# Performance work log

Hardware: AMD Instinct MI355X
Metric: run time of the kernel (lower is better)

## Reference

```python
import jax, jax.numpy as jnp
import numpy as np
from jax import lax


def setup_inputs() -> dict:
    key = jax.random.key(0)
    k1, k2, k3 = jax.random.split(key, 3)
    B, H, W_, C = 2, 384, 1280, 3
    F = 32
    return {
        "xl": jax.random.normal(k1, (B, H, W_, C), dtype=jnp.float32),
        "xr": jax.random.normal(k2, (B, H, W_, C), dtype=jnp.float32),
        "W": jax.random.normal(k3, (3, 3, C, F), dtype=jnp.float32) * 0.1,
        "b": jnp.zeros((F,), dtype=jnp.float32),
        "num_disparity": 96,
    }


def _features(x, W, b):
    # stand-in for the pretrained backbone: 3x3 stride-2 conv + relu (channels_last)
    f = lax.conv_general_dilated(x, W, window_strides=(2, 2), padding="SAME",
                                 dimension_numbers=("NHWC", "HWIO", "NHWC"))
    return jax.nn.relu(f + b)


def reference(xl, xr, W, b, num_disparity):
    D = num_disparity
    x = jnp.concatenate([xl, xr], axis=0)            # [2B,H,W,3]
    f = _features(x, W, b)                            # [2B,H/2,W/2,F]
    f = jax.image.resize(f, (f.shape[0], f.shape[1] * 2, f.shape[2] * 2, f.shape[3]),
                         method="bilinear")          # [2B,H,W,F]
    fl, fr = jnp.split(f, 2, axis=0)                  # each [B,H,W,F]

    # plane-sweep cost volume: sum over channels of squared diff vs width-rolled right features
    def step(_, d):
        cost_d = jnp.sum((fl - jnp.roll(fr, d, axis=2)) ** 2, axis=-1)  # [B,H,W]
        return None, cost_d

    _, cost = lax.scan(step, None, jnp.arange(D))     # [D,B,H,W]

    s = -177.0 * cost / jnp.max(cost, axis=0, keepdims=True)
    w = jax.nn.softmax(s, axis=0)
    disp_idx = jnp.arange(D, dtype=w.dtype)[:, None, None, None]
    return jnp.sum(disp_idx * w, axis=0)              # [B,H,W]
```

## Files before the change

### kernel.cpp

```cpp
#include <hip/hip_runtime.h>
#include <cstddef>

typedef _Float16 h2    __attribute__((ext_vector_type(2)));
typedef _Float16 half8 __attribute__((ext_vector_type(8)));
typedef float    f32x4 __attribute__((ext_vector_type(4)));

#define CH    192
#define CWID  640
#define IMG_H 384
#define IMG_W 1280
#define TW    128
#define GR    224
#define RAWC  179
#define RAWP  192

__device__ __forceinline__ float fastrcp(float x) {
#if __has_builtin(__builtin_amdgcn_rcpf)
  return __builtin_amdgcn_rcpf(x);
#else
  return 1.0f / x;
#endif
}
__device__ __forceinline__ float fastexp2(float x) {
#if __has_builtin(__builtin_amdgcn_exp2f)
  return __builtin_amdgcn_exp2f(x);
#else
  return exp2f(x);
#endif
}
__device__ __forceinline__ float swz16(float x) {
  return __uint_as_float((unsigned)__builtin_amdgcn_ds_swizzle((int)__float_as_uint(x), 0x401F));
}
__device__ __forceinline__ float bperm(int addr, float x) {
  return __uint_as_float((unsigned)__builtin_amdgcn_ds_bpermute(addr, (int)__float_as_uint(x)));
}

__global__ __launch_bounds__(256)
void conv_relu_kernel(const float* __restrict__ xl, const float* __restrict__ xr,
                      const float* __restrict__ Wt, const float* __restrict__ bias,
                      _Float16* __restrict__ Fc) {
  __shared__ float wl[864];
  __shared__ float bl[32];
  const int tid = threadIdx.x;
  for (int t = tid; t < 864; t += 256) wl[t] = Wt[t];
  if (tid < 32) bl[tid] = bias[tid];
  __syncthreads();

  const int g  = blockIdx.x * 256 + tid;
  const int ow = g % CWID;
  const int t2 = g / CWID;
  const int oh = t2 % CH;
  const int bb = t2 / CH;
  const float* src = (bb < 2) ? (xl + (size_t)bb * IMG_H * IMG_W * 3)
                              : (xr + (size_t)(bb - 2) * IMG_H * IMG_W * 3);
  float acc[32];
  #pragma unroll
  for (int c = 0; c < 32; ++c) acc[c] = bl[c];

  #pragma unroll
  for (int kh = 0; kh < 3; ++kh) {
    const int ir = oh * 2 + kh;
    if (ir >= IMG_H) continue;
    #pragma unroll
    for (int kw = 0; kw < 3; ++kw) {
      const int ic = ow * 2 + kw;
      if (ic >= IMG_W) continue;
      const float* px = src + ((size_t)ir * IMG_W + ic) * 3;
      #pragma unroll
      for (int ci = 0; ci < 3; ++ci) {
        const float v = px[ci];
        const float* wp = &wl[((kh * 3 + kw) * 3 + ci) * 32];
        #pragma unroll
        for (int c8 = 0; c8 < 8; ++c8) {
          const float4 w4 = *(const float4*)(wp + c8 * 4);
          acc[c8 * 4 + 0] = fmaf(v, w4.x, acc[c8 * 4 + 0]);
          acc[c8 * 4 + 1] = fmaf(v, w4.y, acc[c8 * 4 + 1]);
          acc[c8 * 4 + 2] = fmaf(v, w4.z, acc[c8 * 4 + 2]);
          acc[c8 * 4 + 3] = fmaf(v, w4.w, acc[c8 * 4 + 3]);
        }
      }
    }
  }
  _Float16 hv[32];
  #pragma unroll
  for (int c = 0; c < 32; ++c) hv[c] = (_Float16)fmaxf(acc[c], 0.f);
  half8* dst = (half8*)(Fc + (size_t)g * 32);
  #pragma unroll
  for (int q = 0; q < 4; ++q) {
    half8 o;
    #pragma unroll
    for (int e = 0; e < 8; ++e) o[e] = hv[q * 8 + e];
    dst[q] = o;
  }
}

__global__ __launch_bounds__(256, 4)
void disparity_mfma_kernel(const _Float16* __restrict__ Fc, float* __restrict__ out) {
  __shared__ alignas(16) _Float16 raw[RAWP * 32];
  __shared__ alignas(16) _Float16 flH[8 * 512];
  __shared__ alignas(16) _Float16 gH[14 * 512];
  __shared__ alignas(16) float As[TW];
  __shared__ alignas(16) float Bs[GR];

  const int tid = threadIdx.x;
  const int w0  = blockIdx.x * TW;
  const int h   = blockIdx.y;
  const int bz  = blockIdx.z;

  const int hk = h >> 1;
  int r0, r1; float wv0;
  if (h & 1) { r0 = hk; r1 = (hk + 1 > CH - 1) ? CH - 1 : hk + 1; wv0 = 0.75f; }
  else       { r0 = (hk - 1 < 0) ? 0 : hk - 1; r1 = hk;           wv0 = 0.25f; }
  const half8 w0v = (half8)(_Float16)wv0;
  const half8 w1v = (half8)(_Float16)(1.0f - wv0);

  const int vbaseL = (w0 >> 1) + 639;
  const int vbaseR = (w0 >> 1) + 592;

  char* const rawB = (char*)raw;

  const char* const bL0 = (const char*)(Fc + ((size_t)bz * CH + r0) * CWID * 32);
  const char* const bL1 = (const char*)(Fc + ((size_t)bz * CH + r1) * CWID * 32);
  const char* const bR0 = (const char*)(Fc + ((size_t)(bz + 2) * CH + r0) * CWID * 32);
  const char* const bR1 = (const char*)(Fc + ((size_t)(bz + 2) * CH + r1) * CWID * 32);

  #pragma unroll
  for (int it = 0; it < 3; ++it) {
    const int task = tid + it * 256;
    const int t    = task >> 2;
    const int tc   = (t > RAWC - 1) ? RAWC - 1 : t;
    const int c16  = task & 3;
    const bool isfl = tc < 66;
    int v = isfl ? (vbaseL + tc) : (vbaseR + tc - 66);
    v -= (v >= 640) ? 640 : 0;
    v -= (v >= 640) ? 640 : 0;
    const char* p0 = isfl ? bL0 : bR0;
    const char* p1 = isfl ? bL1 : bR1;
    const int off = (v << 6) + (c16 << 4);
    const half8 a0 = *(const half8*)(p0 + off);
    const half8 a1 = *(const half8*)(p1 + off);
    const half8 vv = a0 * w0v + a1 * w1v;
    *(half8*)(rawB + t * 64 + ((c16 ^ (t & 3)) << 4)) = vv;
  }
  __syncthreads();

  const _Float16 h75 = (_Float16)0.75f, h25 = (_Float16)0.25f;
  auto row_body = [&](int row) {
    const bool isfl = row < TW;
    const int r  = isfl ? row : row - TW;
    const int uv = isfl ? (w0 + r) : (w0 - 95 + r);
    const int uact = uv < 0 ? uv + IMG_W : (uv >= IMG_W ? uv - IMG_W : uv);
    const int up = uv + IMG_W;
    const int vm0 = (up - 1) >> 1;
    int t0 = vm0 - (isfl ? vbaseL : (vbaseR - 66));
    int t1 = t0 + 1;
    if (uact == 0)         t0 = t1;
    if (uact == IMG_W - 1) t1 = t0;
    const _Float16 hw0 = (up & 1) ? h75 : h25;
    const _Float16 hw1 = (up & 1) ? h25 : h75;
    const half8 h0v = (half8)hw0;
    const half8 h1v = (half8)hw1;
    const char* r0p = rawB + t0 * 64;
    const char* r1p = rawB + t1 * 64;
    const int k0s = t0 & 3, k1s = t1 & 3;
    const int rr  = r & 15;
    char* dstB = (char*)(isfl ? flH : gH) + (r >> 4) * 1024 + rr * 64;
    float s = 0.f;
    #pragma unroll
    for (int c16 = 0; c16 < 4; ++c16) {
      const half8 a = *(const half8*)(r0p + ((c16 ^ k0s) << 4));
      const half8 b = *(const half8*)(r1p + ((c16 ^ k1s) << 4));
      const half8 v = a * h0v + b * h1v;
      #pragma unroll
      for (int e = 0; e < 4; ++e) {
        h2 pe = {v[2 * e], v[2 * e + 1]};
#if __has_builtin(__builtin_amdgcn_fdot2)
        s = __builtin_amdgcn_fdot2(pe, pe, s, false);
#else
        s += (float)pe[0] * (float)pe[0] + (float)pe[1] * (float)pe[1];
#endif
      }
      *(half8*)(dstB + ((c16 ^ (rr & 3)) << 4)) = v;
    }
    if (isfl) As[r] = s; else Bs[r] = s;
  };
  row_body(tid);
  if (tid < TW + GR - 256) row_body(tid + 256);
  __syncthreads();

  const int lane = tid & 63;
  const int wid  = tid >> 6;
  const int n  = lane & 15;
  const int gq = lane >> 4;
  const int foffB = n * 64 + ((gq ^ (n & 3)) << 4);
  const int bpaddr = (lane ^ 32) << 2;

  #pragma unroll
  for (int pp = 0; pp < 2; ++pp) {
    const int p = wid * 2 + pp;
    const half8 bfrag = *(const half8*)((const char*)flH + p * 1024 + foffB);
    f32x4 acc[7];
    #pragma unroll
    for (int dq = 0; dq < 7; ++dq) {
      const half8 afrag = *(const half8*)((const char*)gH + (p + dq) * 1024 + foffB);
      f32x4 z = {0.f, 0.f, 0.f, 0.f};
      acc[dq] = __builtin_amdgcn_mfma_f32_16x16x32_f16(afrag, bfrag, z, 0, 0, 0);
    }

    const float Ai = As[p * 16 + n];
    float cv[7][4];
    float mn = 3.0e38f, mx = -3.0e38f;
    #pragma unroll
    for (int dq = 0; dq < 7; ++dq) {
      const f32x4 b4 = *(const f32x4*)(&Bs[(p + dq) * 16 + gq * 4]);
      float cm[4], cx[4];
      #pragma unroll
      for (int rg = 0; rg < 4; ++rg) {
        const int m = gq * 4 + rg;
        const float cc = fmaf(-2.f, acc[dq][rg], Ai + b4[rg]);
        const bool valid = (dq != 0 || m >= n) && (dq != 6 || m < n);
        cm[rg] = valid ? cc : 3.0e38f;
        cx[rg] = valid ? cc : -3.0e38f;
        cv[dq][rg] = cm[rg];
      }
      mn = fminf(mn, fminf(fminf(cm[0], cm[1]), fminf(cm[2], cm[3])));
      mx = fmaxf(mx, fmaxf(fmaxf(cx[0], cx[1]), fmaxf(cx[2], cx[3])));
    }
    mn = fminf(mn, swz16(mn));
    mx = fmaxf(mx, swz16(mx));
    mn = fminf(mn, bperm(bpaddr, mn));
    mx = fmaxf(mx, bperm(bpaddr, mx));

    const float ralpha = 177.0f * 1.4426950408889634f * fastrcp(mx);
    const float na   = -ralpha;
    const float base = ralpha * mn;
    float sw0 = 0.f, sdw0 = 0.f, sw1 = 0.f, sdw1 = 0.f;
    #pragma unroll
    for (int dq = 0; dq < 7; ++dq) {
      #pragma unroll
      for (int rg = 0; rg < 4; ++rg) {
        const int m = gq * 4 + rg;
        const float wgt = fastexp2(fmaf(na, cv[dq][rg], base));
        const float kf = (float)(95 - (dq * 16 + m - n));
        if (rg & 2) { sw1 += wgt; sdw1 = fmaf(kf, wgt, sdw1); }
        else        { sw0 += wgt; sdw0 = fmaf(kf, wgt, sdw0); }
      }
    }
    float sw = sw0 + sw1, sdw = sdw0 + sdw1;
    sw  += swz16(sw);
    sdw += swz16(sdw);
    sw  += bperm(bpaddr, sw);
    sdw += bperm(bpaddr, sdw);
    if (gq == 0)
      out[((size_t)bz * IMG_H + h) * IMG_W + w0 + p * 16 + n] = sdw * fastrcp(sw);
  }
}

extern "C" void kernel_launch(void* const* d_in, const int* in_sizes, int n_in,
                              void* d_out, int out_size, void* d_ws, size_t ws_size,
                              hipStream_t stream) {
  (void)in_sizes; (void)n_in; (void)out_size; (void)ws_size;
  const float* xl   = (const float*)d_in[0];
  const float* xr   = (const float*)d_in[1];
  const float* Wt   = (const float*)d_in[2];
  const float* bias = (const float*)d_in[3];
  _Float16* Fc = (_Float16*)d_ws;
  float* out = (float*)d_out;

  hipLaunchKernelGGL(conv_relu_kernel, dim3(1920), dim3(256), 0, stream,
                     xl, xr, Wt, bias, Fc);
  hipLaunchKernelGGL(disparity_mfma_kernel, dim3(IMG_W / TW, IMG_H, 2), dim3(256), 0, stream,
                     Fc, out);
}
```

Before: 78.68 us.

## Split raw staging into channel halves and pack softmax math with packed-f32 ops

```diff
diff --git a/kernel.cpp b/kernel.cpp
--- a/kernel.cpp
+++ b/kernel.cpp
@@ -4,6 +4,7 @@
 typedef _Float16 h2    __attribute__((ext_vector_type(2)));
 typedef _Float16 half8 __attribute__((ext_vector_type(8)));
 typedef float    f32x4 __attribute__((ext_vector_type(4)));
+typedef float    f32x2 __attribute__((ext_vector_type(2)));
 
 #define CH    192
 #define CWID  640
@@ -34,6 +35,20 @@
 __device__ __forceinline__ float bperm(int addr, float x) {
   return __uint_as_float((unsigned)__builtin_amdgcn_ds_bpermute(addr, (int)__float_as_uint(x)));
 }
+__device__ __forceinline__ f32x2 pkadd(f32x2 a, f32x2 b) {
+  f32x2 d; asm("v_pk_add_f32 %0, %1, %2" : "=v"(d) : "v"(a), "v"(b)); return d;
+}
+__device__ __forceinline__ f32x2 pkfma(f32x2 a, f32x2 b, f32x2 c) {
+  f32x2 d; asm("v_pk_fma_f32 %0, %1, %2, %3" : "=v"(d) : "v"(a), "v"(b), "v"(c)); return d;
+}
+__device__ __forceinline__ float min3f(float a, float b, float c) {
+  float d; asm("v_min3_f32 %0, %1, %2, %3" : "=v"(d) : "v"(a), "v"(b), "v"(c)); return d;
+}
+__device__ __forceinline__ float max3f(float a, float b, float c) {
+  float d; asm("v_max3_f32 %0, %1, %2, %3" : "=v"(d) : "v"(a), "v"(b), "v"(c)); return d;
+}
+__device__ __forceinline__ f32x2 lo2(f32x4 v) { f32x2 r; r.x = v.x; r.y = v.y; return r; }
+__device__ __forceinline__ f32x2 hi2(f32x4 v) { f32x2 r; r.x = v.z; r.y = v.w; return r; }
 
 __global__ __launch_bounds__(256)
 void conv_relu_kernel(const float* __restrict__ xl, const float* __restrict__ xr,
@@ -96,7 +111,7 @@
 
 __global__ __launch_bounds__(256, 4)
 void disparity_mfma_kernel(const _Float16* __restrict__ Fc, float* __restrict__ out) {
-  __shared__ alignas(16) _Float16 raw[RAWP * 32];
+  __shared__ alignas(16) _Float16 raw[RAWP * 16];
   __shared__ alignas(16) _Float16 flH[8 * 512];
   __shared__ alignas(16) _Float16 gH[14 * 512];
   __shared__ alignas(16) float As[TW];
@@ -124,28 +139,11 @@
   const char* const bR0 = (const char*)(Fc + ((size_t)(bz + 2) * CH + r0) * CWID * 32);
   const char* const bR1 = (const char*)(Fc + ((size_t)(bz + 2) * CH + r1) * CWID * 32);
 
-  #pragma unroll
-  for (int it = 0; it < 3; ++it) {
-    const int task = tid + it * 256;
-    const int t    = task >> 2;
-    const int tc   = (t > RAWC - 1) ? RAWC - 1 : t;
-    const int c16  = task & 3;
-    const bool isfl = tc < 66;
-    int v = isfl ? (vbaseL + tc) : (vbaseR + tc - 66);
-    v -= (v >= 640) ? 640 : 0;
-    v -= (v >= 640) ? 640 : 0;
-    const char* p0 = isfl ? bL0 : bR0;
-    const char* p1 = isfl ? bL1 : bR1;
-    const int off = (v << 6) + (c16 << 4);
-    const half8 a0 = *(const half8*)(p0 + off);
-    const half8 a1 = *(const half8*)(p1 + off);
-    const half8 vv = a0 * w0v + a1 * w1v;
-    *(half8*)(rawB + t * 64 + ((c16 ^ (t & 3)) << 4)) = vv;
-  }
-  __syncthreads();
-
   const _Float16 h75 = (_Float16)0.75f, h25 = (_Float16)0.25f;
-  auto row_body = [&](int row) {
+  int a_r0off, a_s0, a_r1off, a_s1, a_swz; half8 a_h0, a_h1; char* a_dst;
+  int b_r0off, b_s0, b_r1off, b_s1, b_swz; half8 b_h0, b_h1; char* b_dst;
+  {
+    const int row = tid;
     const bool isfl = row < TW;
     const int r  = isfl ? row : row - TW;
     const int uv = isfl ? (w0 + r) : (w0 - 95 + r);
@@ -156,36 +154,96 @@
     int t1 = t0 + 1;
     if (uact == 0)         t0 = t1;
     if (uact == IMG_W - 1) t1 = t0;
-    const _Float16 hw0 = (up & 1) ? h75 : h25;
-    const _Float16 hw1 = (up & 1) ? h25 : h75;
-    const half8 h0v = (half8)hw0;
-    const half8 h1v = (half8)hw1;
-    const char* r0p = rawB + t0 * 64;
-    const char* r1p = rawB + t1 * 64;
-    const int k0s = t0 & 3, k1s = t1 & 3;
-    const int rr  = r & 15;
-    char* dstB = (char*)(isfl ? flH : gH) + (r >> 4) * 1024 + rr * 64;
-    float s = 0.f;
-    #pragma unroll
-    for (int c16 = 0; c16 < 4; ++c16) {
-      const half8 a = *(const half8*)(r0p + ((c16 ^ k0s) << 4));
-      const half8 b = *(const half8*)(r1p + ((c16 ^ k1s) << 4));
-      const half8 v = a * h0v + b * h1v;
-      #pragma unroll
-      for (int e = 0; e < 4; ++e) {
-        h2 pe = {v[2 * e], v[2 * e + 1]};
+    a_h0 = (half8)((up & 1) ? h75 : h25);
+    a_h1 = (half8)((up & 1) ? h25 : h75);
+    a_r0off = t0 * 32; a_s0 = (t0 & 1) << 4;
+    a_r1off = t1 * 32; a_s1 = (t1 & 1) << 4;
+    a_swz = r & 3;
+    a_dst = (char*)(isfl ? flH : gH) + (r >> 4) * 1024 + (r & 15) * 64;
+  }
+  {
+    const int row = tid + 256;
+    const int r  = row - TW;
+    const int uv = w0 - 95 + r;
+    const int uact = uv < 0 ? uv + IMG_W : (uv >= IMG_W ? uv - IMG_W : uv);
+    const int up = uv + IMG_W;
+    const int vm0 = (up - 1) >> 1;
+    int t0 = vm0 - (vbaseR - 66);
+    int t1 = t0 + 1;
+    if (uact == 0)         t0 = t1;
+    if (uact == IMG_W - 1) t1 = t0;
+    b_h0 = (half8)((up & 1) ? h75 : h25);
+    b_h1 = (half8)((up & 1) ? h25 : h75);
+    b_r0off = t0 * 32; b_s0 = (t0 & 1) << 4;
+    b_r1off = t1 * 32; b_s1 = (t1 & 1) << 4;
+    b_swz = r & 3;
+    b_dst = (char*)gH + (r >> 4) * 1024 + (r & 15) * 64;
+  }
+
+  float sA = 0.f, sB = 0.f;
+  #pragma unroll
+  for (int half = 0; half < 2; ++half) {
+    #pragma unroll
+    for (int it = 0; it < 2; ++it) {
+      const int task = tid + it * 256;
+      if (it == 0 || tid < 128) {
+        const int t    = task >> 1;
+        const int cpos = task & 1;
+        const int tc   = (t > RAWC - 1) ? RAWC - 1 : t;
+        const bool isfl = tc < 66;
+        int v = isfl ? (vbaseL + tc) : (vbaseR + tc - 66);
+        v -= (v >= 640) ? 640 : 0;
+        v -= (v >= 640) ? 640 : 0;
+        const char* p0 = isfl ? bL0 : bR0;
+        const char* p1 = isfl ? bL1 : bR1;
+        const int off = (v << 6) + ((half * 2 + cpos) << 4);
+        const half8 a0 = *(const half8*)(p0 + off);
+        const half8 a1 = *(const half8*)(p1 + off);
+        const half8 vv = a0 * w0v + a1 * w1v;
+        *(half8*)(rawB + t * 32 + ((cpos ^ (t & 1)) << 4)) = vv;
+      }
+    }
+    __syncthreads();
+
+    #pragma unroll
+    for (int cpos = 0; cpos < 2; ++cpos) {
+      const int c16 = half * 2 + cpos;
+      const int cb  = cpos << 4;
+      {
+        const half8 a = *(const half8*)(rawB + a_r0off + (cb ^ a_s0));
+        const half8 b = *(const half8*)(rawB + a_r1off + (cb ^ a_s1));
+        const half8 v = a * a_h0 + b * a_h1;
+        #pragma unroll
+        for (int e = 0; e < 4; ++e) {
+          h2 pe = {v[2 * e], v[2 * e + 1]};
 #if __has_builtin(__builtin_amdgcn_fdot2)
-        s = __builtin_amdgcn_fdot2(pe, pe, s, false);
+          sA = __builtin_amdgcn_fdot2(pe, pe, sA, false);
 #else
-        s += (float)pe[0] * (float)pe[0] + (float)pe[1] * (float)pe[1];
+          sA += (float)pe[0] * (float)pe[0] + (float)pe[1] * (float)pe[1];
 #endif
-      }
-      *(half8*)(dstB + ((c16 ^ (rr & 3)) << 4)) = v;
-    }
-    if (isfl) As[r] = s; else Bs[r] = s;
-  };
-  row_body(tid);
-  if (tid < TW + GR - 256) row_body(tid + 256);
+        }
+        *(half8*)(a_dst + ((c16 ^ a_swz) << 4)) = v;
+      }
+      if (tid < TW + GR - 256) {
+        const half8 a = *(const half8*)(rawB + b_r0off + (cb ^ b_s0));
+        const half8 b = *(const half8*)(rawB + b_r1off + (cb ^ b_s1));
+        const half8 v = a * b_h0 + b * b_h1;
+        #pragma unroll
+        for (int e = 0; e < 4; ++e) {
+          h2 pe = {v[2 * e], v[2 * e + 1]};
+#if __has_builtin(__builtin_amdgcn_fdot2)
+          sB = __builtin_amdgcn_fdot2(pe, pe, sB, false);
+#else
+          sB += (float)pe[0] * (float)pe[0] + (float)pe[1] * (float)pe[1];
+#endif
+        }
+        *(half8*)(b_dst + ((c16 ^ b_swz) << 4)) = v;
+      }
+    }
+    __syncthreads();
+  }
+  if (tid < TW) As[tid] = sA; else Bs[tid - TW] = sA;
+  if (tid < TW + GR - 256) Bs[tid + 256 - TW] = sB;
   __syncthreads();
 
   const int lane = tid & 63;
@@ -194,6 +252,7 @@
   const int gq = lane >> 4;
   const int foffB = n * 64 + ((gq ^ (n & 3)) << 4);
   const int bpaddr = (lane ^ 32) << 2;
+  const float Cbase = (float)(95 - 4 * gq + n);
 
   #pragma unroll
   for (int pp = 0; pp < 2; ++pp) {
@@ -208,23 +267,34 @@
     }
 
     const float Ai = As[p * 16 + n];
-    float cv[7][4];
+    f32x2 AiP; AiP.x = Ai; AiP.y = Ai;
+    f32x2 m2P; m2P.x = -2.f; m2P.y = -2.f;
     float mn = 3.0e38f, mx = -3.0e38f;
     #pragma unroll
     for (int dq = 0; dq < 7; ++dq) {
       const f32x4 b4 = *(const f32x4*)(&Bs[(p + dq) * 16 + gq * 4]);
-      float cm[4], cx[4];
-      #pragma unroll
-      for (int rg = 0; rg < 4; ++rg) {
-        const int m = gq * 4 + rg;
-        const float cc = fmaf(-2.f, acc[dq][rg], Ai + b4[rg]);
-        const bool valid = (dq != 0 || m >= n) && (dq != 6 || m < n);
-        cm[rg] = valid ? cc : 3.0e38f;
-        cx[rg] = valid ? cc : -3.0e38f;
-        cv[dq][rg] = cm[rg];
-      }
-      mn = fminf(mn, fminf(fminf(cm[0], cm[1]), fminf(cm[2], cm[3])));
-      mx = fmaxf(mx, fmaxf(fmaxf(cx[0], cx[1]), fmaxf(cx[2], cx[3])));
+      f32x2 c01 = pkfma(m2P, lo2(acc[dq]), pkadd(AiP, lo2(b4)));
+      f32x2 c23 = pkfma(m2P, hi2(acc[dq]), pkadd(AiP, hi2(b4)));
+      if (dq == 0 || dq == 6) {
+        float e0 = c01.x, e1 = c01.y, e2 = c23.x, e3 = c23.y;
+        const bool v0 = (dq == 0) ? (gq * 4 + 0 >= n) : (gq * 4 + 0 < n);
+        const bool v1 = (dq == 0) ? (gq * 4 + 1 >= n) : (gq * 4 + 1 < n);
+        const bool v2 = (dq == 0) ? (gq * 4 + 2 >= n) : (gq * 4 + 2 < n);
+        const bool v3 = (dq == 0) ? (gq * 4 + 3 >= n) : (gq * 4 + 3 < n);
+        mx = max3f(mx, v0 ? e0 : -3.0e38f, v1 ? e1 : -3.0e38f);
+        mx = max3f(mx, v2 ? e2 : -3.0e38f, v3 ? e3 : -3.0e38f);
+        c01.x = v0 ? e0 : 3.0e38f;  c01.y = v1 ? e1 : 3.0e38f;
+        c23.x = v2 ? e2 : 3.0e38f;  c23.y = v3 ? e3 : 3.0e38f;
+        mn = min3f(mn, c01.x, c01.y);
+        mn = min3f(mn, c23.x, c23.y);
+      } else {
+        mn = min3f(mn, c01.x, c01.y);
+        mn = min3f(mn, c23.x, c23.y);
+        mx = max3f(mx, c01.x, c01.y);
+        mx = max3f(mx, c23.x, c23.y);
+      }
+      acc[dq].x = c01.x; acc[dq].y = c01.y;
+      acc[dq].z = c23.x; acc[dq].w = c23.y;
     }
     mn = fminf(mn, swz16(mn));
     mx = fmaxf(mx, swz16(mx));
@@ -234,19 +304,27 @@
     const float ralpha = 177.0f * 1.4426950408889634f * fastrcp(mx);
     const float na   = -ralpha;
     const float base = ralpha * mn;
-    float sw0 = 0.f, sdw0 = 0.f, sw1 = 0.f, sdw1 = 0.f;
+    f32x2 naP;   naP.x = na;   naP.y = na;
+    f32x2 baseP; baseP.x = base; baseP.y = base;
+    float sw0 = 0.f, sw1 = 0.f, sw2 = 0.f, sw3 = 0.f;
+    float sk0 = 0.f, sk1 = 0.f, sk2 = 0.f, sk3 = 0.f;
     #pragma unroll
     for (int dq = 0; dq < 7; ++dq) {
-      #pragma unroll
-      for (int rg = 0; rg < 4; ++rg) {
-        const int m = gq * 4 + rg;
-        const float wgt = fastexp2(fmaf(na, cv[dq][rg], base));
-        const float kf = (float)(95 - (dq * 16 + m - n));
-        if (rg & 2) { sw1 += wgt; sdw1 = fmaf(kf, wgt, sdw1); }
-        else        { sw0 += wgt; sdw0 = fmaf(kf, wgt, sdw0); }
-      }
-    }
-    float sw = sw0 + sw1, sdw = sdw0 + sdw1;
+      const f32x2 g01 = pkfma(naP, lo2(acc[dq]), baseP);
+      const f32x2 g23 = pkfma(naP, hi2(acc[dq]), baseP);
+      const float w0_ = fastexp2(g01.x);
+      const float w1_ = fastexp2(g01.y);
+      const float w2_ = fastexp2(g23.x);
+      const float w3_ = fastexp2(g23.y);
+      sw0 += w0_; sw1 += w1_; sw2 += w2_; sw3 += w3_;
+      sk0 = fmaf((float)(16 * dq + 0), w0_, sk0);
+      sk1 = fmaf((float)(16 * dq + 1), w1_, sk1);
+      sk2 = fmaf((float)(16 * dq + 2), w2_, sk2);
+      sk3 = fmaf((float)(16 * dq + 3), w3_, sk3);
+    }
+    float sw  = (sw0 + sw1) + (sw2 + sw3);
+    float skw = (sk0 + sk1) + (sk2 + sk3);
+    float sdw = fmaf(Cbase, sw, -skw);
     sw  += swz16(sw);
     sdw += swz16(sdw);
     sw  += bperm(bpaddr, sw);
```

Result: faster. 77.07 us (-2.0%).
